# Kernel optimization log

Hardware: AMD Instinct MI355X
Metric: run time of the kernel (lower is better)

Reference implementation:

```python
import jax, jax.numpy as jnp
import numpy as np

IN_C = 256
OUT_C = 256
HID = IN_C * 2
N_POINTS = 262144
N_NODES = 8192
B = 16
MAX_NODES = 512
EPS = 1e-5


def _mlp(h, w1, b1, g1, be1, w2, b2):
    # PyG MLP([C, 2C, out], norm='layer_norm'): lin -> layernorm -> relu -> (dropout, eval=identity) -> lin
    h = h @ w1 + b1
    mu = jnp.mean(h, axis=-1, keepdims=True)
    var = jnp.var(h, axis=-1, keepdims=True)
    h = (h - mu) * jax.lax.rsqrt(var + EPS) * g1 + be1
    h = jax.nn.relu(h)
    return h @ w2 + b2


def setup_inputs() -> dict:
    key = jax.random.key(0)
    ks = jax.random.split(key, 16)
    x = jax.random.normal(ks[0], (N_POINTS, IN_C), dtype=jnp.float32)
    f_point_batches = jnp.sort(jax.random.randint(ks[1], (N_POINTS,), 0, N_NODES)).astype(jnp.int32)
    # equal-sized graphs (16 graphs x 512 nodes), sorted as torch.split/pad_sequence assume
    g_node_batches = jnp.repeat(jnp.arange(B, dtype=jnp.int32), MAX_NODES)
    s = 1.0 / np.sqrt(IN_C)
    s2 = 1.0 / np.sqrt(HID)
    def lin(k, fan_in, shape, scale):
        return jax.random.uniform(k, shape, jnp.float32, -scale, scale)
    params = {}
    for i, name in enumerate(['Wq', 'Wk']):
        base = 2 + i * 6
        params[f'{name}_w1'] = lin(ks[base + 0], IN_C, (IN_C, HID), s)
        params[f'{name}_b1'] = lin(ks[base + 1], IN_C, (HID,), s)
        params[f'{name}_g1'] = jnp.ones((HID,), jnp.float32)
        params[f'{name}_be1'] = jnp.zeros((HID,), jnp.float32)
        params[f'{name}_w2'] = lin(ks[base + 2], HID, (HID, OUT_C), s2)
        params[f'{name}_b2'] = lin(ks[base + 3], HID, (OUT_C,), s2)
    return dict(x=x, f_point_batches=f_point_batches, g_node_batches=g_node_batches,
                num_graphs=B, max_nodes=MAX_NODES, **params)


def reference(x, f_point_batches, g_node_batches, num_graphs, max_nodes,
              Wq_w1, Wq_b1, Wq_g1, Wq_be1, Wq_w2, Wq_b2,
              Wk_w1, Wk_b1, Wk_g1, Wk_be1, Wk_w2, Wk_b2):
    n_nodes = g_node_batches.shape[0]
    C = x.shape[1]
    # scatter_mean over points -> per-node feature means [n_nodes, C]
    sums = jax.ops.segment_sum(x, f_point_batches, num_segments=n_nodes)
    cnt = jax.ops.segment_sum(jnp.ones((x.shape[0],), x.dtype), f_point_batches, num_segments=n_nodes)
    mean = sums / jnp.maximum(cnt, 1.0)[:, None]
    # ragged split by graph + pad_sequence -> [B, max_nodes, C]
    starts = jnp.searchsorted(g_node_batches, jnp.arange(num_graphs, dtype=g_node_batches.dtype))
    pos = jnp.arange(n_nodes) - starts[g_node_batches]
    padded = jnp.zeros((num_graphs, max_nodes, C), x.dtype).at[g_node_batches, pos].set(mean, mode='drop')
    q = _mlp(padded, Wq_w1, Wq_b1, Wq_g1, Wq_be1, Wq_w2, Wq_b2)  # [B, MAXN, out]
    k = _mlp(padded, Wk_w1, Wk_b1, Wk_g1, Wk_be1, Wk_w2, Wk_b2)
    return jnp.einsum('bnd,bmd->bnm', q, k)  # bmm(q, k^T)
```

## Files before the change

kernel.cpp:

```cpp
#include <hip/hip_runtime.h>
#include <hip/hip_bf16.h>

#define N_POINTS 262144
#define N_NODES  8192
#define IN_C     256
#define HID      512
#define OUT_C    256
#define NB       16
#define MAXN     512
#define EPSV     1e-5f
#define NPB      32

typedef __attribute__((ext_vector_type(8))) short short8;
typedef __attribute__((ext_vector_type(4))) float f32x4;
typedef __attribute__((ext_vector_type(4))) float f4v;
#define MFMA16(a, b, c) __builtin_amdgcn_mfma_f32_16x16x32_bf16((a), (b), (c), 0, 0, 0)


__global__ __launch_bounds__(256) void prelude_k(
    const int* __restrict__ fpb, int* __restrict__ starts,
    const float* __restrict__ W1q, const float* __restrict__ W1k,
    const float* __restrict__ W2q, const float* __restrict__ W2k,
    __hip_bfloat16* __restrict__ P1q, __hip_bfloat16* __restrict__ P1k,
    __hip_bfloat16* __restrict__ P2q, __hip_bfloat16* __restrict__ P2k)
{
  if (blockIdx.x < 1024) {
    const int i = blockIdx.x * 256 + threadIdx.x;
    const int cur = fpb[i];
    const int prev = (i == 0) ? -1 : fpb[i - 1];
    for (int n = prev + 1; n <= cur; ++n) starts[n] = i;
    if (i == N_POINTS - 1)
      for (int n = cur + 1; n <= N_NODES; ++n) starts[n] = N_POINTS;
    return;
  }
  const int bid = blockIdx.x - 1024;
  const int sel = bid >> 6;
  const float* W; __hip_bfloat16* P; int N;
  switch (sel) {
    case 0:  W = W1q; P = P1q; N = HID;   break;
    case 1:  W = W1k; P = P1k; N = HID;   break;
    case 2:  W = W2q; P = P2q; N = OUT_C; break;
    default: W = W2k; P = P2k; N = OUT_C; break;
  }
  const int idx = (bid & 63) * 256 + threadIdx.x;
  const int NF = N >> 4;
  const int lane = idx & 63;
  const int nf = (idx >> 6) % NF;
  const int ks = idx / (64 * NF);
  const int k0 = ks * 32 + (lane >> 4) * 8;
  const int n  = nf * 16 + (lane & 15);
  __hip_bfloat16 tmp[8];
  #pragma unroll
  for (int j = 0; j < 8; ++j) tmp[j] = __float2bfloat16(W[(size_t)(k0 + j) * N + n]);
  *(uint4*)(P + (size_t)idx * 8) = *(uint4*)tmp;
}

__device__ __forceinline__ void accum_rows(
    const float* __restrict__ x, int lo, int hi, int l,
    f4v& a0, f4v& a1, f4v& a2, f4v& a3)
{
  int r = lo;
  for (; r + 4 <= hi; r += 4) {
    f4v v0 = *(const f4v*)(x + (size_t)(r + 0) * IN_C + l * 4);
    f4v v1 = *(const f4v*)(x + (size_t)(r + 1) * IN_C + l * 4);
    f4v v2 = *(const f4v*)(x + (size_t)(r + 2) * IN_C + l * 4);
    f4v v3 = *(const f4v*)(x + (size_t)(r + 3) * IN_C + l * 4);
    a0 += v0; a1 += v1; a2 += v2; a3 += v3;
  }
  for (; r < hi; ++r)
    a0 += *(const f4v*)(x + (size_t)r * IN_C + l * 4);
}

__global__ __launch_bounds__(256) void scatter_mean_k(
    const float* __restrict__ x, const int* __restrict__ starts,
    __hip_bfloat16* __restrict__ mean)
{
  const int node = blockIdx.x * 4 + (threadIdx.x >> 6);
  const int l = threadIdx.x & 63;
  const int s_ = starts[node], e_ = starts[node + 1];
  f4v a0 = (f4v)0.f, a1 = (f4v)0.f, a2 = (f4v)0.f, a3 = (f4v)0.f;
  accum_rows(x, s_, e_, l, a0, a1, a2, a3);
  a0 += a1 + a2 + a3;
  const int cnt = e_ - s_;
  const float inv = cnt > 0 ? 1.0f / (float)cnt : 0.0f;
  __hip_bfloat16 o[4];
  o[0] = __float2bfloat16(a0.x * inv);
  o[1] = __float2bfloat16(a0.y * inv);
  o[2] = __float2bfloat16(a0.z * inv);
  o[3] = __float2bfloat16(a0.w * inv);
  *(uint2*)(mean + (size_t)node * IN_C + l * 4) = *(uint2*)o;
}

__global__ __launch_bounds__(1024, 4) void mlp_k(
    const __hip_bfloat16* __restrict__ mean,
    const __hip_bfloat16* __restrict__ P1q, const __hip_bfloat16* __restrict__ P2q,
    const float* __restrict__ b1q, const float* __restrict__ g1q,
    const float* __restrict__ be1q, const float* __restrict__ b2q,
    const __hip_bfloat16* __restrict__ P1k, const __hip_bfloat16* __restrict__ P2k,
    const float* __restrict__ b1k, const float* __restrict__ g1k,
    const float* __restrict__ be1k, const float* __restrict__ b2k,
    __hip_bfloat16* __restrict__ qo, __hip_bfloat16* __restrict__ ko)
{
  const int n0 = blockIdx.x * NPB;
  const int t = threadIdx.x;
  const int w = t >> 6, l = t & 63, lg = l >> 4, lm = l & 15;
  const int h = w >> 3;
  const int c = w & 7;

  const __hip_bfloat16* P1 = h ? P1k : P1q;
  const __hip_bfloat16* P2 = h ? P2k : P2q;
  const float* b1  = h ? b1k  : b1q;
  const float* g1  = h ? g1k  : g1q;
  const float* be1 = h ? be1k : be1q;
  const float* b2  = h ? b2k  : b2q;
  __hip_bfloat16* out = h ? ko : qo;

  __shared__ __hip_bfloat16 As[NPB * 264];
  __shared__ __hip_bfloat16 Hs[2][NPB * 520];
  __shared__ float lnp[16][NPB][2];
  __hip_bfloat16* Hsh = Hs[h];

  {
    const int nl = t >> 5, c8 = (t & 31) * 8;
    uint4 v = *(const uint4*)(mean + (size_t)(n0 + nl) * IN_C + c8);
    *(uint4*)(As + nl * 264 + c8) = v;
  }
  __syncthreads();

  f32x4 acc1[2][4];
  #pragma unroll
  for (int mi = 0; mi < 2; ++mi)
    #pragma unroll
    for (int nj = 0; nj < 4; ++nj)
      #pragma unroll
      for (int r = 0; r < 4; ++r) acc1[mi][nj][r] = 0.f;

  short8 bcur[4], bnxt[4];
  {
    const __hip_bfloat16* bp = P1 + ((size_t)(c * 4) * 64 + l) * 8;
    #pragma unroll
    for (int nj = 0; nj < 4; ++nj) bcur[nj] = *(const short8*)(bp + (size_t)nj * 512);
  }
  for (int ks = 0; ks < 8; ++ks) {
    if (ks < 7) {
      const __hip_bfloat16* bp = P1 + ((size_t)((ks + 1) * 32 + c * 4) * 64 + l) * 8;
      #pragma unroll
      for (int nj = 0; nj < 4; ++nj) bnxt[nj] = *(const short8*)(bp + (size_t)nj * 512);
    }
    short8 a0 = *(const short8*)(As + lm * 264 + ks * 32 + lg * 8);
    short8 a1 = *(const short8*)(As + (16 + lm) * 264 + ks * 32 + lg * 8);
    #pragma unroll
    for (int nj = 0; nj < 4; ++nj) {
      acc1[0][nj] = MFMA16(a0, bcur[nj], acc1[0][nj]);
      acc1[1][nj] = MFMA16(a1, bcur[nj], acc1[1][nj]);
    }
    #pragma unroll
    for (int nj = 0; nj < 4; ++nj) bcur[nj] = bnxt[nj];
  }

  float b1v[4], g1v[4], e1v[4];
  #pragma unroll
  for (int nj = 0; nj < 4; ++nj) {
    const int col = c * 64 + nj * 16 + lm;
    b1v[nj] = b1[col]; g1v[nj] = g1[col]; e1v[nj] = be1[col];
  }
  #pragma unroll
  for (int mi = 0; mi < 2; ++mi)
    #pragma unroll
    for (int nj = 0; nj < 4; ++nj)
      #pragma unroll
      for (int r = 0; r < 4; ++r) acc1[mi][nj][r] += b1v[nj];

  #pragma unroll
  for (int mi = 0; mi < 2; ++mi)
    #pragma unroll
    for (int r = 0; r < 4; ++r) {
      float s = 0.f, q = 0.f;
      #pragma unroll
      for (int nj = 0; nj < 4; ++nj) {
        const float v = acc1[mi][nj][r];
        s += v; q += v * v;
      }
      #pragma unroll
      for (int off = 1; off < 16; off <<= 1) {
        s += __shfl_xor(s, off);
        q += __shfl_xor(q, off);
      }
      if (lm == 0) {
        const int row = mi * 16 + lg * 4 + r;
        lnp[w][row][0] = s;
        lnp[w][row][1] = q;
      }
    }
  __syncthreads();

  #pragma unroll
  for (int mi = 0; mi < 2; ++mi)
    #pragma unroll
    for (int r = 0; r < 4; ++r) {
      const int row = mi * 16 + lg * 4 + r;
      float S = 0.f, Q = 0.f;
      #pragma unroll
      for (int w2 = 0; w2 < 8; ++w2) {
        S += lnp[h * 8 + w2][row][0];
        Q += lnp[h * 8 + w2][row][1];
      }
      const float mu = S * (1.0f / HID);
      const float rs = rsqrtf(Q * (1.0f / HID) - mu * mu + EPSV);
      #pragma unroll
      for (int nj = 0; nj < 4; ++nj) {
        const float y = (acc1[mi][nj][r] - mu) * rs * g1v[nj] + e1v[nj];
        Hsh[row * 520 + c * 64 + nj * 16 + lm] = __float2bfloat16(fmaxf(y, 0.f));
      }
    }
  __syncthreads();

  f32x4 acc2[2][2];
  #pragma unroll
  for (int mi = 0; mi < 2; ++mi)
    #pragma unroll
    for (int nj = 0; nj < 2; ++nj)
      #pragma unroll
      for (int r = 0; r < 4; ++r) acc2[mi][nj][r] = 0.f;

  short8 b2cur[2], b2nxt[2];
  {
    const __hip_bfloat16* bp = P2 + ((size_t)(c * 2) * 64 + l) * 8;
    #pragma unroll
    for (int nj = 0; nj < 2; ++nj) b2cur[nj] = *(const short8*)(bp + (size_t)nj * 512);
  }
  for (int ks = 0; ks < 16; ++ks) {
    if (ks < 15) {
      const __hip_bfloat16* bp = P2 + ((size_t)((ks + 1) * 16 + c * 2) * 64 + l) * 8;
      #pragma unroll
      for (int nj = 0; nj < 2; ++nj) b2nxt[nj] = *(const short8*)(bp + (size_t)nj * 512);
    }
    short8 a0 = *(const short8*)(Hsh + lm * 520 + ks * 32 + lg * 8);
    short8 a1 = *(const short8*)(Hsh + (16 + lm) * 520 + ks * 32 + lg * 8);
    #pragma unroll
    for (int nj = 0; nj < 2; ++nj) {
      acc2[0][nj] = MFMA16(a0, b2cur[nj], acc2[0][nj]);
      acc2[1][nj] = MFMA16(a1, b2cur[nj], acc2[1][nj]);
    }
    #pragma unroll
    for (int nj = 0; nj < 2; ++nj) b2cur[nj] = b2nxt[nj];
  }

  float b2v[2];
  #pragma unroll
  for (int nj = 0; nj < 2; ++nj) b2v[nj] = b2[c * 32 + nj * 16 + lm];
  #pragma unroll
  for (int mi = 0; mi < 2; ++mi)
    #pragma unroll
    for (int nj = 0; nj < 2; ++nj)
      #pragma unroll
      for (int r = 0; r < 4; ++r) {
        const int row = n0 + mi * 16 + lg * 4 + r;
        const int col = c * 32 + nj * 16 + lm;
        out[(size_t)row * OUT_C + col] = __float2bfloat16(acc2[mi][nj][r] + b2v[nj]);
      }
}

__global__ __launch_bounds__(256, 4) void bmm_k(
    const __hip_bfloat16* __restrict__ q, const __hip_bfloat16* __restrict__ k,
    float* __restrict__ out)
{
  const int b  = blockIdx.z;
  const int n0 = blockIdx.x * 64;
  const int m0 = blockIdx.y * 64;
  const int t = threadIdx.x;
  const int w = t >> 6, l = t & 63, lg = l >> 4, lm = l & 15;

  const __hip_bfloat16* qb = q + ((size_t)b * MAXN + n0 + w * 16) * OUT_C;
  const __hip_bfloat16* kb = k + ((size_t)b * MAXN + m0) * OUT_C;

  f32x4 acc[4];
  #pragma unroll
  for (int nj = 0; nj < 4; ++nj)
    #pragma unroll
    for (int r = 0; r < 4; ++r) acc[nj][r] = 0.f;

  for (int ks = 0; ks < 8; ++ks) {
    short8 a = *(const short8*)(qb + (size_t)lm * OUT_C + ks * 32 + lg * 8);
    #pragma unroll
    for (int nj = 0; nj < 4; ++nj) {
      short8 bb = *(const short8*)(kb + (size_t)(nj * 16 + lm) * OUT_C + ks * 32 + lg * 8);
      acc[nj] = MFMA16(a, bb, acc[nj]);
    }
  }

  #pragma unroll
  for (int nj = 0; nj < 4; ++nj)
    #pragma unroll
    for (int r = 0; r < 4; ++r) {
      const int nrow = n0 + w * 16 + lg * 4 + r;
      const int mcol = m0 + nj * 16 + lm;
      out[((size_t)b * MAXN + nrow) * MAXN + mcol] = acc[nj][r];
    }
}

extern "C" void kernel_launch(void* const* d_in, const int* in_sizes, int n_in,
                              void* d_out, int out_size, void* d_ws, size_t ws_size,
                              hipStream_t stream)
{
  const float* x   = (const float*)d_in[0];
  const int*   fpb = (const int*)d_in[1];
  const float* Wq_w1  = (const float*)d_in[5];
  const float* Wq_b1  = (const float*)d_in[6];
  const float* Wq_g1  = (const float*)d_in[7];
  const float* Wq_be1 = (const float*)d_in[8];
  const float* Wq_w2  = (const float*)d_in[9];
  const float* Wq_b2  = (const float*)d_in[10];
  const float* Wk_w1  = (const float*)d_in[11];
  const float* Wk_b1  = (const float*)d_in[12];
  const float* Wk_g1  = (const float*)d_in[13];
  const float* Wk_be1 = (const float*)d_in[14];
  const float* Wk_w2  = (const float*)d_in[15];
  const float* Wk_b2  = (const float*)d_in[16];

  __hip_bfloat16* ws = (__hip_bfloat16*)d_ws;
  __hip_bfloat16* P1q  = ws;
  __hip_bfloat16* P1k  = P1q + 131072;
  __hip_bfloat16* P2q  = P1k + 131072;
  __hip_bfloat16* P2k  = P2q + 131072;
  __hip_bfloat16* mean = P2k + 131072;
  __hip_bfloat16* qo   = mean + 2097152;
  __hip_bfloat16* ko   = qo + 2097152;
  int* starts = (int*)(ko + 2097152);
  float* out = (float*)d_out;

  prelude_k<<<1280, 256, 0, stream>>>(fpb, starts,
      Wq_w1, Wk_w1, Wq_w2, Wk_w2, P1q, P1k, P2q, P2k);
  scatter_mean_k<<<N_NODES / 4, 256, 0, stream>>>(x, starts, mean);
  mlp_k<<<N_NODES / NPB, 1024, 0, stream>>>(
      mean, P1q, P2q, Wq_b1, Wq_g1, Wq_be1, Wq_b2,
      P1k, P2k, Wk_b1, Wk_g1, Wk_be1, Wk_b2, qo, ko);
  bmm_k<<<dim3(8, 8, NB), 256, 0, stream>>>(qo, ko, out);
}
```

Measured before the change: 94.75 us.

## Fuse scatter-mean reduction into MLP kernel, computing node means directly into LDS

Removes the separate scatter_mean kernel and its bf16 mean buffer; each wave of the MLP kernel now reduces two nodes' point rows from x and writes the means directly into shared memory. This saves a launch and the global write/read of the mean tensor. In exchange, the bandwidth-heavy reduction now runs inside large 1024-thread blocks with limited occupancy, which may reduce memory-level parallelism during the x streaming phase.

New measurement: 87.94 us. 7.2% less time.

```diff
diff --git a/kernel.cpp b/kernel.cpp
--- a/kernel.cpp
+++ b/kernel.cpp
@@ -55,44 +55,8 @@
   *(uint4*)(P + (size_t)idx * 8) = *(uint4*)tmp;
 }
 
-__device__ __forceinline__ void accum_rows(
-    const float* __restrict__ x, int lo, int hi, int l,
-    f4v& a0, f4v& a1, f4v& a2, f4v& a3)
-{
-  int r = lo;
-  for (; r + 4 <= hi; r += 4) {
-    f4v v0 = *(const f4v*)(x + (size_t)(r + 0) * IN_C + l * 4);
-    f4v v1 = *(const f4v*)(x + (size_t)(r + 1) * IN_C + l * 4);
-    f4v v2 = *(const f4v*)(x + (size_t)(r + 2) * IN_C + l * 4);
-    f4v v3 = *(const f4v*)(x + (size_t)(r + 3) * IN_C + l * 4);
-    a0 += v0; a1 += v1; a2 += v2; a3 += v3;
-  }
-  for (; r < hi; ++r)
-    a0 += *(const f4v*)(x + (size_t)r * IN_C + l * 4);
-}
-
-__global__ __launch_bounds__(256) void scatter_mean_k(
+__global__ __launch_bounds__(1024, 4) void fused_mlp_k(
     const float* __restrict__ x, const int* __restrict__ starts,
-    __hip_bfloat16* __restrict__ mean)
-{
-  const int node = blockIdx.x * 4 + (threadIdx.x >> 6);
-  const int l = threadIdx.x & 63;
-  const int s_ = starts[node], e_ = starts[node + 1];
-  f4v a0 = (f4v)0.f, a1 = (f4v)0.f, a2 = (f4v)0.f, a3 = (f4v)0.f;
-  accum_rows(x, s_, e_, l, a0, a1, a2, a3);
-  a0 += a1 + a2 + a3;
-  const int cnt = e_ - s_;
-  const float inv = cnt > 0 ? 1.0f / (float)cnt : 0.0f;
-  __hip_bfloat16 o[4];
-  o[0] = __float2bfloat16(a0.x * inv);
-  o[1] = __float2bfloat16(a0.y * inv);
-  o[2] = __float2bfloat16(a0.z * inv);
-  o[3] = __float2bfloat16(a0.w * inv);
-  *(uint2*)(mean + (size_t)node * IN_C + l * 4) = *(uint2*)o;
-}
-
-__global__ __launch_bounds__(1024, 4) void mlp_k(
-    const __hip_bfloat16* __restrict__ mean,
     const __hip_bfloat16* __restrict__ P1q, const __hip_bfloat16* __restrict__ P2q,
     const float* __restrict__ b1q, const float* __restrict__ g1q,
     const float* __restrict__ be1q, const float* __restrict__ b2q,
@@ -121,9 +85,58 @@
   __hip_bfloat16* Hsh = Hs[h];
 
   {
-    const int nl = t >> 5, c8 = (t & 31) * 8;
-    uint4 v = *(const uint4*)(mean + (size_t)(n0 + nl) * IN_C + c8);
-    *(uint4*)(As + nl * 264 + c8) = v;
+    const int nodeA = n0 + w * 2;
+    const int sA = starts[nodeA],     eA = starts[nodeA + 1];
+    const int sB = starts[nodeA + 1], eB = starts[nodeA + 2];
+    f4v A0 = (f4v)0.f, A1 = (f4v)0.f, A2 = (f4v)0.f, A3 = (f4v)0.f;
+    f4v B0 = (f4v)0.f, B1 = (f4v)0.f, B2 = (f4v)0.f, B3 = (f4v)0.f;
+    int rA = sA, rB = sB;
+    while (rA + 4 <= eA && rB + 4 <= eB) {
+      f4v a0 = *(const f4v*)(x + (size_t)(rA + 0) * IN_C + l * 4);
+      f4v b0 = *(const f4v*)(x + (size_t)(rB + 0) * IN_C + l * 4);
+      f4v a1 = *(const f4v*)(x + (size_t)(rA + 1) * IN_C + l * 4);
+      f4v b1_ = *(const f4v*)(x + (size_t)(rB + 1) * IN_C + l * 4);
+      f4v a2 = *(const f4v*)(x + (size_t)(rA + 2) * IN_C + l * 4);
+      f4v b2_ = *(const f4v*)(x + (size_t)(rB + 2) * IN_C + l * 4);
+      f4v a3 = *(const f4v*)(x + (size_t)(rA + 3) * IN_C + l * 4);
+      f4v b3_ = *(const f4v*)(x + (size_t)(rB + 3) * IN_C + l * 4);
+      A0 += a0; B0 += b0; A1 += a1; B1 += b1_;
+      A2 += a2; B2 += b2_; A3 += a3; B3 += b3_;
+      rA += 4; rB += 4;
+    }
+    for (; rA + 4 <= eA; rA += 4) {
+      f4v v0 = *(const f4v*)(x + (size_t)(rA + 0) * IN_C + l * 4);
+      f4v v1 = *(const f4v*)(x + (size_t)(rA + 1) * IN_C + l * 4);
+      f4v v2 = *(const f4v*)(x + (size_t)(rA + 2) * IN_C + l * 4);
+      f4v v3 = *(const f4v*)(x + (size_t)(rA + 3) * IN_C + l * 4);
+      A0 += v0; A1 += v1; A2 += v2; A3 += v3;
+    }
+    for (; rA < eA; ++rA) A0 += *(const f4v*)(x + (size_t)rA * IN_C + l * 4);
+    for (; rB + 4 <= eB; rB += 4) {
+      f4v v0 = *(const f4v*)(x + (size_t)(rB + 0) * IN_C + l * 4);
+      f4v v1 = *(const f4v*)(x + (size_t)(rB + 1) * IN_C + l * 4);
+      f4v v2 = *(const f4v*)(x + (size_t)(rB + 2) * IN_C + l * 4);
+      f4v v3 = *(const f4v*)(x + (size_t)(rB + 3) * IN_C + l * 4);
+      B0 += v0; B1 += v1; B2 += v2; B3 += v3;
+    }
+    for (; rB < eB; ++rB) B0 += *(const f4v*)(x + (size_t)rB * IN_C + l * 4);
+
+    A0 += A1 + A2 + A3;
+    B0 += B1 + B2 + B3;
+    const int cntA = eA - sA, cntB = eB - sB;
+    const float invA = cntA > 0 ? 1.0f / (float)cntA : 0.0f;
+    const float invB = cntB > 0 ? 1.0f / (float)cntB : 0.0f;
+    __hip_bfloat16 oA[4], oB[4];
+    oA[0] = __float2bfloat16(A0.x * invA);
+    oA[1] = __float2bfloat16(A0.y * invA);
+    oA[2] = __float2bfloat16(A0.z * invA);
+    oA[3] = __float2bfloat16(A0.w * invA);
+    oB[0] = __float2bfloat16(B0.x * invB);
+    oB[1] = __float2bfloat16(B0.y * invB);
+    oB[2] = __float2bfloat16(B0.z * invB);
+    oB[3] = __float2bfloat16(B0.w * invB);
+    *(uint2*)(As + (w * 2 + 0) * 264 + l * 4) = *(uint2*)oA;
+    *(uint2*)(As + (w * 2 + 1) * 264 + l * 4) = *(uint2*)oB;
   }
   __syncthreads();
 
@@ -135,27 +148,27 @@
       #pragma unroll
       for (int r = 0; r < 4; ++r) acc1[mi][nj][r] = 0.f;
 
-  short8 bcur[4], bnxt[4];
   {
-    const __hip_bfloat16* bp = P1 + ((size_t)(c * 4) * 64 + l) * 8;
-    #pragma unroll
-    for (int nj = 0; nj < 4; ++nj) bcur[nj] = *(const short8*)(bp + (size_t)nj * 512);
-  }
-  for (int ks = 0; ks < 8; ++ks) {
-    if (ks < 7) {
-      const __hip_bfloat16* bp = P1 + ((size_t)((ks + 1) * 32 + c * 4) * 64 + l) * 8;
-      #pragma unroll
-      for (int nj = 0; nj < 4; ++nj) bnxt[nj] = *(const short8*)(bp + (size_t)nj * 512);
-    }
-    short8 a0 = *(const short8*)(As + lm * 264 + ks * 32 + lg * 8);
-    short8 a1 = *(const short8*)(As + (16 + lm) * 264 + ks * 32 + lg * 8);
-    #pragma unroll
-    for (int nj = 0; nj < 4; ++nj) {
-      acc1[0][nj] = MFMA16(a0, bcur[nj], acc1[0][nj]);
-      acc1[1][nj] = MFMA16(a1, bcur[nj], acc1[1][nj]);
-    }
-    #pragma unroll
-    for (int nj = 0; nj < 4; ++nj) bcur[nj] = bnxt[nj];
+    short8 bcur[4], bnxt[4];
+    const __hip_bfloat16* bp0 = P1 + ((size_t)(c * 4) * 64 + l) * 8;
+    #pragma unroll
+    for (int nj = 0; nj < 4; ++nj) bcur[nj] = *(const short8*)(bp0 + (size_t)nj * 512);
+    for (int ks = 0; ks < 8; ++ks) {
+      if (ks < 7) {
+        const __hip_bfloat16* bp = P1 + ((size_t)((ks + 1) * 32 + c * 4) * 64 + l) * 8;
+        #pragma unroll
+        for (int nj = 0; nj < 4; ++nj) bnxt[nj] = *(const short8*)(bp + (size_t)nj * 512);
+      }
+      short8 a0 = *(const short8*)(As + lm * 264 + ks * 32 + lg * 8);
+      short8 a1 = *(const short8*)(As + (16 + lm) * 264 + ks * 32 + lg * 8);
+      #pragma unroll
+      for (int nj = 0; nj < 4; ++nj) {
+        acc1[0][nj] = MFMA16(a0, bcur[nj], acc1[0][nj]);
+        acc1[1][nj] = MFMA16(a1, bcur[nj], acc1[1][nj]);
+      }
+      #pragma unroll
+      for (int nj = 0; nj < 4; ++nj) bcur[nj] = bnxt[nj];
+    }
   }
 
   float b1v[4], g1v[4], e1v[4];
@@ -223,27 +236,27 @@
       #pragma unroll
       for (int r = 0; r < 4; ++r) acc2[mi][nj][r] = 0.f;
 
-  short8 b2cur[2], b2nxt[2];
   {
-    const __hip_bfloat16* bp = P2 + ((size_t)(c * 2) * 64 + l) * 8;
-    #pragma unroll
-    for (int nj = 0; nj < 2; ++nj) b2cur[nj] = *(const short8*)(bp + (size_t)nj * 512);
-  }
-  for (int ks = 0; ks < 16; ++ks) {
-    if (ks < 15) {
-      const __hip_bfloat16* bp = P2 + ((size_t)((ks + 1) * 16 + c * 2) * 64 + l) * 8;
-      #pragma unroll
-      for (int nj = 0; nj < 2; ++nj) b2nxt[nj] = *(const short8*)(bp + (size_t)nj * 512);
-    }
-    short8 a0 = *(const short8*)(Hsh + lm * 520 + ks * 32 + lg * 8);
-    short8 a1 = *(const short8*)(Hsh + (16 + lm) * 520 + ks * 32 + lg * 8);
-    #pragma unroll
-    for (int nj = 0; nj < 2; ++nj) {
-      acc2[0][nj] = MFMA16(a0, b2cur[nj], acc2[0][nj]);
-      acc2[1][nj] = MFMA16(a1, b2cur[nj], acc2[1][nj]);
-    }
-    #pragma unroll
-    for (int nj = 0; nj < 2; ++nj) b2cur[nj] = b2nxt[nj];
+    short8 bcur[2], bnxt[2];
+    const __hip_bfloat16* bp0 = P2 + ((size_t)(c * 2) * 64 + l) * 8;
+    #pragma unroll
+    for (int nj = 0; nj < 2; ++nj) bcur[nj] = *(const short8*)(bp0 + (size_t)nj * 512);
+    for (int ks = 0; ks < 16; ++ks) {
+      if (ks < 15) {
+        const __hip_bfloat16* bp = P2 + ((size_t)((ks + 1) * 16 + c * 2) * 64 + l) * 8;
+        #pragma unroll
+        for (int nj = 0; nj < 2; ++nj) bnxt[nj] = *(const short8*)(bp + (size_t)nj * 512);
+      }
+      short8 a0 = *(const short8*)(Hsh + lm * 520 + ks * 32 + lg * 8);
+      short8 a1 = *(const short8*)(Hsh + (16 + lm) * 520 + ks * 32 + lg * 8);
+      #pragma unroll
+      for (int nj = 0; nj < 2; ++nj) {
+        acc2[0][nj] = MFMA16(a0, bcur[nj], acc2[0][nj]);
+        acc2[1][nj] = MFMA16(a1, bcur[nj], acc2[1][nj]);
+      }
+      #pragma unroll
+      for (int nj = 0; nj < 2; ++nj) bcur[nj] = bnxt[nj];
+    }
   }
 
   float b2v[2];
@@ -323,17 +336,15 @@
   __hip_bfloat16* P1k  = P1q + 131072;
   __hip_bfloat16* P2q  = P1k + 131072;
   __hip_bfloat16* P2k  = P2q + 131072;
-  __hip_bfloat16* mean = P2k + 131072;
-  __hip_bfloat16* qo   = mean + 2097152;
+  __hip_bfloat16* qo   = P2k + 131072;
   __hip_bfloat16* ko   = qo + 2097152;
   int* starts = (int*)(ko + 2097152);
   float* out = (float*)d_out;
 
   prelude_k<<<1280, 256, 0, stream>>>(fpb, starts,
       Wq_w1, Wk_w1, Wq_w2, Wk_w2, P1q, P1k, P2q, P2k);
-  scatter_mean_k<<<N_NODES / 4, 256, 0, stream>>>(x, starts, mean);
-  mlp_k<<<N_NODES / NPB, 1024, 0, stream>>>(
-      mean, P1q, P2q, Wq_b1, Wq_g1, Wq_be1, Wq_b2,
+  fused_mlp_k<<<N_NODES / NPB, 1024, 0, stream>>>(
+      x, starts, P1q, P2q, Wq_b1, Wq_g1, Wq_be1, Wq_b2,
       P1k, P2k, Wk_b1, Wk_g1, Wk_be1, Wk_b2, qo, ko);
   bmm_k<<<dim3(8, 8, NB), 256, 0, stream>>>(qo, ko, out);
 }
```
